# Optimization experiments

Measured on AMD Instinct MI355X. Metric: run time of the kernel, lower is better.

## Reference

```python
import jax, jax.numpy as jnp
import numpy as np

N_NODES = 50000
N_EDGES = 800000
IN_C = 128
OUT_C = 128


def setup_inputs() -> dict:
    key = jax.random.key(0)
    k1, k2, k3 = jax.random.split(key, 3)
    x = jax.random.normal(k1, (N_NODES, IN_C), dtype=jnp.float32)
    edge_index = jax.random.randint(k2, (2, N_EDGES), 0, N_NODES, dtype=jnp.int64)
    weight = jax.random.normal(k3, (IN_C, OUT_C), dtype=jnp.float32) * 0.01
    bias = jnp.zeros((OUT_C,), dtype=jnp.float32)
    return {"x": x, "edge_index": edge_index, "weight": weight, "bias": bias}


def reference(x, edge_index, weight, bias):
    num_nodes = x.shape[0]
    # add self-loops
    loop = jnp.arange(num_nodes, dtype=edge_index.dtype)
    src = jnp.concatenate([edge_index[0], loop])  # [E + N]
    dst = jnp.concatenate([edge_index[1], loop])  # [E + N]
    # in-degree (incl. self-loops) via scatter-add
    deg = jax.ops.segment_sum(jnp.ones_like(dst, dtype=x.dtype), dst,
                              num_segments=num_nodes)
    # deg >= 1 due to self-loops, but guard inf like the original
    deg_inv_sqrt = jnp.where(deg > 0, jax.lax.rsqrt(deg), 0.0)
    norm = deg_inv_sqrt[src] * deg_inv_sqrt[dst]  # [E + N]
    x_transformed = x @ weight  # [N, out_c]
    messages = x_transformed[src] * norm[:, None]  # [E + N, out_c]
    out = jax.ops.segment_sum(messages, dst, num_segments=num_nodes)
    return out + bias
```

## Files before the change

kernel.cpp:

```cpp
#include <hip/hip_runtime.h>

#define C 128
#define CHUNK 3200
#define K4CAP 5120

typedef short bf16x8 __attribute__((ext_vector_type(8)));
typedef float f32x4 __attribute__((ext_vector_type(4)));

__device__ inline unsigned short f2bf(float f) {
    unsigned u = __float_as_uint(f);
    u += 0x7fffu + ((u >> 16) & 1u);
    return (unsigned short)(u >> 16);
}

__device__ inline unsigned pk2bf(float lo, float hi) {
    return (unsigned)f2bf(lo) | ((unsigned)f2bf(hi) << 16);
}

__global__ __launch_bounds__(256) void kfused(
        const int* __restrict__ ei, int e,
        int* __restrict__ cur, unsigned* __restrict__ staging,
        int nblocks, int nbuck,
        const float* __restrict__ W, unsigned short* __restrict__ Wt) {
    int b = blockIdx.x;
    int t = threadIdx.x;
    if (b >= nblocks) {
        int i = (b - nblocks) * 256 + t;
        int nn = i >> 7, k = i & 127;
        Wt[nn * 128 + k] = f2bf(W[k * 128 + nn]);
        return;
    }
    __shared__ int sdst[CHUNK];
    __shared__ int ssrc[CHUNK];
    __shared__ int h[256];
    __shared__ int c[256];
    h[t] = 0;
    __syncthreads();
    int base = b * CHUNK;
    int lim = min(CHUNK, e - base);
    for (int i = t; i < lim; i += 256) {
        int s = ei[base + i];
        int d = ei[e + base + i];
        ssrc[i] = s;
        sdst[i] = d;
        atomicAdd(&h[d >> 8], 1);
    }
    __syncthreads();
    if (t < nbuck) {
        int cnt = h[t];
        c[t] = cnt ? atomicAdd(&cur[t], cnt) : 0;
    }
    __syncthreads();
    for (int i = t; i < lim; i += 256) {
        int s = ssrc[i];
        int d = sdst[i];
        int g = d >> 8;
        int pos = atomicAdd(&c[g], 1);
        if (pos < K4CAP)
            staging[(size_t)g * K4CAP + pos] = (unsigned)s | ((unsigned)(d & 255) << 16);
    }
}

__global__ __launch_bounds__(256) void k4_finalize(
        const unsigned* __restrict__ staging, const int* __restrict__ cur,
        int2* __restrict__ row_se, float* __restrict__ dis,
        unsigned short* __restrict__ srcs, int n) {
    __shared__ unsigned rec[K4CAP];
    __shared__ int sc[256];
    __shared__ int cu[256];
    int g = blockIdx.x, t = threadIdx.x;
    int cnt = min(cur[g], K4CAP);
    int s0 = g * K4CAP;
    sc[t] = 0;
    __syncthreads();
    for (int li = t; li < cnt; li += 256) {
        unsigned r = staging[s0 + li];
        rec[li] = r;
        atomicAdd(&sc[r >> 16], 1);
    }
    __syncthreads();
    int v = sc[t];
    __syncthreads();
    for (int off = 1; off < 256; off <<= 1) {
        int u = (t >= off) ? sc[t - off] : 0;
        __syncthreads();
        sc[t] += u;
        __syncthreads();
    }
    int excl = sc[t] - v;
    int idx = g * 256 + t;
    if (idx < n) {
        row_se[idx] = make_int2(s0 + excl, s0 + excl + v);
        dis[idx] = rsqrtf((float)(v + 1));
    }
    cu[t] = s0 + excl;
    __syncthreads();
    for (int li = t; li < cnt; li += 256) {
        unsigned r = rec[li];
        int pos = atomicAdd(&cu[r >> 16], 1);
        srcs[pos] = (unsigned short)(r & 0xffffu);
    }
}

__global__ __launch_bounds__(256) void gemm_mfma(
        const float* __restrict__ x, const unsigned short* __restrict__ Wt,
        const float* __restrict__ dis, unsigned short* __restrict__ xts, int n) {
    const int lane = threadIdx.x & 63;
    const int wave = threadIdx.x >> 6;
    const int m = lane & 15;
    const int q = lane >> 4;
    const int r0 = blockIdx.x * 64 + wave * 16;
    const int row = r0 + m;
    const int rowc = (row < n) ? row : (n - 1);

    f32x4 acc[8];
#pragma unroll
    for (int nt = 0; nt < 8; ++nt) acc[nt] = (f32x4){0.f, 0.f, 0.f, 0.f};

#pragma unroll
    for (int kb = 0; kb < 4; ++kb) {
        const int k0 = kb * 32 + q * 8;
        const float4* xp = (const float4*)(x + (size_t)rowc * 128 + k0);
        float4 xa = xp[0];
        float4 xb = xp[1];
        union { unsigned u[4]; bf16x8 v; } af;
        af.u[0] = pk2bf(xa.x, xa.y);
        af.u[1] = pk2bf(xa.z, xa.w);
        af.u[2] = pk2bf(xb.x, xb.y);
        af.u[3] = pk2bf(xb.z, xb.w);
#pragma unroll
        for (int nt = 0; nt < 8; ++nt) {
            bf16x8 bf = *(const bf16x8*)(Wt + (size_t)(nt * 16 + m) * 128 + k0);
            acc[nt] = __builtin_amdgcn_mfma_f32_16x16x32_bf16(af.v, bf, acc[nt], 0, 0, 0);
        }
    }

    float dv[4];
    int gr[4];
#pragma unroll
    for (int r = 0; r < 4; ++r) {
        gr[r] = r0 + q * 4 + r;
        dv[r] = dis[(gr[r] < n) ? gr[r] : (n - 1)];
    }
#pragma unroll
    for (int nt = 0; nt < 8; ++nt) {
        int col = nt * 16 + m;
#pragma unroll
        for (int r = 0; r < 4; ++r) {
            if (gr[r] < n)
                xts[(size_t)gr[r] * 128 + col] = f2bf(acc[nt][r] * dv[r]);
        }
    }
}

__device__ inline void acc8(float* a, uint4 w) {
    a[0] += __uint_as_float(w.x << 16);
    a[1] += __uint_as_float(w.x & 0xffff0000u);
    a[2] += __uint_as_float(w.y << 16);
    a[3] += __uint_as_float(w.y & 0xffff0000u);
    a[4] += __uint_as_float(w.z << 16);
    a[5] += __uint_as_float(w.z & 0xffff0000u);
    a[6] += __uint_as_float(w.w << 16);
    a[7] += __uint_as_float(w.w & 0xffff0000u);
}

__global__ void gather4(const int2* __restrict__ row_se,
                        const unsigned short* __restrict__ srcs,
                        const unsigned short* __restrict__ xts,
                        const float* __restrict__ dis,
                        const float* __restrict__ bias, float* __restrict__ out, int n) {
    int node = blockIdx.x * 4 + (threadIdx.x >> 6);
    if (node >= n) return;
    int lane = threadIdx.x & 63;
    int e = lane >> 4, q = lane & 15;
    const uint4* x4 = (const uint4*)xts;
    int2 se = row_se[node];
    int end = se.y;
    float a0[8] = {0, 0, 0, 0, 0, 0, 0, 0};
    float a1[8] = {0, 0, 0, 0, 0, 0, 0, 0};
    if (e == 0) acc8(a0, x4[node * 16 + q]);
    int j = se.x + e;
    for (; j + 4 < end; j += 8) {
        int s0 = srcs[j], s1 = srcs[j + 4];
        uint4 m0 = x4[s0 * 16 + q];
        uint4 m1 = x4[s1 * 16 + q];
        acc8(a0, m0);
        acc8(a1, m1);
    }
    if (j < end) acc8(a0, x4[(int)srcs[j] * 16 + q]);
#pragma unroll
    for (int i = 0; i < 8; ++i) a0[i] += a1[i];
#pragma unroll
    for (int i = 0; i < 8; ++i) {
        a0[i] += __shfl_xor(a0[i], 16, 64);
        a0[i] += __shfl_xor(a0[i], 32, 64);
    }
    float d = dis[node];
    if (e == 0) {
        const float4 b = ((const float4*)bias)[q * 2];
        float4 o;
        o.x = a0[0] * d + b.x;
        o.y = a0[1] * d + b.y;
        o.z = a0[2] * d + b.z;
        o.w = a0[3] * d + b.w;
        ((float4*)(out + (size_t)node * 128))[q * 2] = o;
    } else if (e == 1) {
        const float4 b = ((const float4*)bias)[q * 2 + 1];
        float4 o;
        o.x = a0[4] * d + b.x;
        o.y = a0[5] * d + b.y;
        o.z = a0[6] * d + b.z;
        o.w = a0[7] * d + b.w;
        ((float4*)(out + (size_t)node * 128))[q * 2 + 1] = o;
    }
}

extern "C" void kernel_launch(void* const* d_in, const int* in_sizes, int n_in,
                              void* d_out, int out_size, void* d_ws, size_t ws_size,
                              hipStream_t stream) {
    const float* x    = (const float*)d_in[0];
    const int*   ei   = (const int*)d_in[1];
    const float* W    = (const float*)d_in[2];
    const float* bias = (const float*)d_in[3];
    float* out = (float*)d_out;

    const int n = in_sizes[0] / C;
    const int e = in_sizes[1] / 2;
    const int nblocks = (e + CHUNK - 1) / CHUNK;
    const int nbuck = (n + 255) >> 8;
    const int G = (n + 63) / 64;

    char* p = (char*)d_ws;
    auto alloc = [&](size_t bytes) {
        char* r = p;
        p += (bytes + 15) & ~(size_t)15;
        return (void*)r;
    };
    int*      cur     = (int*)alloc(nbuck * 4);
    unsigned* staging = (unsigned*)alloc((size_t)nbuck * K4CAP * 4);
    int2*     row_se  = (int2*)alloc((size_t)n * 8);
    float*    dis     = (float*)alloc(n * 4);
    unsigned short* srcs = (unsigned short*)alloc((size_t)nbuck * K4CAP * 2);
    unsigned short* xts  = (unsigned short*)alloc((size_t)n * C * 2);
    unsigned short* Wt   = (unsigned short*)alloc(128 * 128 * 2);

    hipMemsetAsync(cur, 0, nbuck * 4, stream);
    kfused<<<nblocks + 64, 256, 0, stream>>>(ei, e, cur, staging, nblocks,
                                             nbuck, W, Wt);
    k4_finalize<<<nbuck, 256, 0, stream>>>(staging, cur, row_se, dis, srcs, n);
    gemm_mfma<<<G, 256, 0, stream>>>(x, Wt, dis, xts, n);
    gather4<<<(n + 3) / 4, 256, 0, stream>>>(row_se, srcs, xts, dis, bias, out, n);
}
```

Measured before the change: 161.8 us.

## Fuse CSR finalize with GEMM and drop global atomics via per-block slots

The bucketing kernel now writes each block's per-bucket counts into fixed-size slots instead of reserving space through global atomics, which removes the memset launch. The finalize and GEMM kernels are merged into one launch with disjoint block ranges, so the GEMM no longer waits on degree computation. Because of that, the source-side normalization moves out of the GEMM epilogue and into the gather loop, which adds one dis load per edge. Risks: slots hold at most 64 edges per bucket per block, edges past that are silently dropped, and finalize threads copy their slots serially.

```diff
diff --git a/kernel.cpp b/kernel.cpp
--- a/kernel.cpp
+++ b/kernel.cpp
@@ -2,6 +2,7 @@
 
 #define C 128
 #define CHUNK 3200
+#define SLOT 64
 #define K4CAP 5120
 
 typedef short bf16x8 __attribute__((ext_vector_type(8)));
@@ -17,9 +18,9 @@
     return (unsigned)f2bf(lo) | ((unsigned)f2bf(hi) << 16);
 }
 
-__global__ __launch_bounds__(256) void kfused(
+__global__ __launch_bounds__(256) void kA(
         const int* __restrict__ ei, int e,
-        int* __restrict__ cur, unsigned* __restrict__ staging,
+        int* __restrict__ cnt, unsigned* __restrict__ staging,
         int nblocks, int nbuck,
         const float* __restrict__ W, unsigned short* __restrict__ Wt) {
     int b = blockIdx.x;
@@ -47,8 +48,8 @@
     }
     __syncthreads();
     if (t < nbuck) {
-        int cnt = h[t];
-        c[t] = cnt ? atomicAdd(&cur[t], cnt) : 0;
+        cnt[t * nblocks + b] = h[t];
+        c[t] = (t * nblocks + b) * SLOT;
     }
     __syncthreads();
     for (int i = t; i < lim; i += 256) {
@@ -56,112 +57,120 @@
         int d = sdst[i];
         int g = d >> 8;
         int pos = atomicAdd(&c[g], 1);
-        if (pos < K4CAP)
-            staging[(size_t)g * K4CAP + pos] = (unsigned)s | ((unsigned)(d & 255) << 16);
-    }
-}
-
-__global__ __launch_bounds__(256) void k4_finalize(
-        const unsigned* __restrict__ staging, const int* __restrict__ cur,
+        if (pos < (g * nblocks + b + 1) * SLOT)
+            staging[pos] = (unsigned)s | ((unsigned)(d & 255) << 16);
+    }
+}
+
+__global__ __launch_bounds__(256) void kB(
+        const unsigned* __restrict__ staging, const int* __restrict__ cnt,
+        int nblocks, int nbuck,
         int2* __restrict__ row_se, float* __restrict__ dis,
-        unsigned short* __restrict__ srcs, int n) {
+        unsigned short* __restrict__ srcs,
+        const float* __restrict__ x, const unsigned short* __restrict__ Wt,
+        unsigned short* __restrict__ xts, int n) {
     __shared__ unsigned rec[K4CAP];
     __shared__ int sc[256];
     __shared__ int cu[256];
-    int g = blockIdx.x, t = threadIdx.x;
-    int cnt = min(cur[g], K4CAP);
-    int s0 = g * K4CAP;
-    sc[t] = 0;
-    __syncthreads();
-    for (int li = t; li < cnt; li += 256) {
-        unsigned r = staging[s0 + li];
-        rec[li] = r;
-        atomicAdd(&sc[r >> 16], 1);
-    }
-    __syncthreads();
-    int v = sc[t];
-    __syncthreads();
-    for (int off = 1; off < 256; off <<= 1) {
-        int u = (t >= off) ? sc[t - off] : 0;
-        __syncthreads();
-        sc[t] += u;
-        __syncthreads();
-    }
-    int excl = sc[t] - v;
-    int idx = g * 256 + t;
-    if (idx < n) {
-        row_se[idx] = make_int2(s0 + excl, s0 + excl + v);
-        dis[idx] = rsqrtf((float)(v + 1));
-    }
-    cu[t] = s0 + excl;
-    __syncthreads();
-    for (int li = t; li < cnt; li += 256) {
-        unsigned r = rec[li];
-        int pos = atomicAdd(&cu[r >> 16], 1);
-        srcs[pos] = (unsigned short)(r & 0xffffu);
-    }
-}
-
-__global__ __launch_bounds__(256) void gemm_mfma(
-        const float* __restrict__ x, const unsigned short* __restrict__ Wt,
-        const float* __restrict__ dis, unsigned short* __restrict__ xts, int n) {
-    const int lane = threadIdx.x & 63;
-    const int wave = threadIdx.x >> 6;
-    const int m = lane & 15;
-    const int q = lane >> 4;
-    const int r0 = blockIdx.x * 64 + wave * 16;
-    const int row = r0 + m;
-    const int rowc = (row < n) ? row : (n - 1);
-
-    f32x4 acc[8];
-#pragma unroll
-    for (int nt = 0; nt < 8; ++nt) acc[nt] = (f32x4){0.f, 0.f, 0.f, 0.f};
-
-#pragma unroll
-    for (int kb = 0; kb < 4; ++kb) {
-        const int k0 = kb * 32 + q * 8;
-        const float4* xp = (const float4*)(x + (size_t)rowc * 128 + k0);
-        float4 xa = xp[0];
-        float4 xb = xp[1];
-        union { unsigned u[4]; bf16x8 v; } af;
-        af.u[0] = pk2bf(xa.x, xa.y);
-        af.u[1] = pk2bf(xa.z, xa.w);
-        af.u[2] = pk2bf(xb.x, xb.y);
-        af.u[3] = pk2bf(xb.z, xb.w);
+    int b = blockIdx.x, t = threadIdx.x;
+    if (b < nbuck) {
+        int g = b;
+        int segc = (t < nblocks) ? cnt[g * nblocks + t] : 0;
+        sc[t] = segc;
+        __syncthreads();
+        for (int off = 1; off < 256; off <<= 1) {
+            int u = (t >= off) ? sc[t - off] : 0;
+            __syncthreads();
+            sc[t] += u;
+            __syncthreads();
+        }
+        int segbase = sc[t] - segc;
+        int total = min(sc[255], K4CAP);
+        const unsigned* segp = staging + ((size_t)g * nblocks + t) * SLOT;
+        for (int k = 0; k < segc; ++k)
+            if (segbase + k < K4CAP) rec[segbase + k] = segp[k];
+        __syncthreads();
+        sc[t] = 0;
+        __syncthreads();
+        for (int li = t; li < total; li += 256)
+            atomicAdd(&sc[rec[li] >> 16], 1);
+        __syncthreads();
+        int v = sc[t];
+        __syncthreads();
+        for (int off = 1; off < 256; off <<= 1) {
+            int u = (t >= off) ? sc[t - off] : 0;
+            __syncthreads();
+            sc[t] += u;
+            __syncthreads();
+        }
+        int excl = sc[t] - v;
+        int idx = g * 256 + t;
+        int s0 = g * K4CAP;
+        if (idx < n) {
+            row_se[idx] = make_int2(s0 + excl, s0 + excl + v);
+            dis[idx] = rsqrtf((float)(v + 1));
+        }
+        cu[t] = s0 + excl;
+        __syncthreads();
+        for (int li = t; li < total; li += 256) {
+            unsigned r = rec[li];
+            int pos = atomicAdd(&cu[r >> 16], 1);
+            srcs[pos] = (unsigned short)(r & 0xffffu);
+        }
+    } else {
+        const int gb = b - nbuck;
+        const int lane = t & 63;
+        const int wave = t >> 6;
+        const int m = lane & 15;
+        const int q = lane >> 4;
+        const int r0 = gb * 64 + wave * 16;
+        const int row = r0 + m;
+        const int rowc = (row < n) ? row : (n - 1);
+
+        f32x4 acc[8];
+#pragma unroll
+        for (int nt = 0; nt < 8; ++nt) acc[nt] = (f32x4){0.f, 0.f, 0.f, 0.f};
+
+#pragma unroll
+        for (int kb = 0; kb < 4; ++kb) {
+            const int k0 = kb * 32 + q * 8;
+            const float4* xp = (const float4*)(x + (size_t)rowc * 128 + k0);
+            float4 xa = xp[0];
+            float4 xb = xp[1];
+            union { unsigned u[4]; bf16x8 v; } af;
+            af.u[0] = pk2bf(xa.x, xa.y);
+            af.u[1] = pk2bf(xa.z, xa.w);
+            af.u[2] = pk2bf(xb.x, xb.y);
+            af.u[3] = pk2bf(xb.z, xb.w);
+#pragma unroll
+            for (int nt = 0; nt < 8; ++nt) {
+                bf16x8 bf = *(const bf16x8*)(Wt + (size_t)(nt * 16 + m) * 128 + k0);
+                acc[nt] = __builtin_amdgcn_mfma_f32_16x16x32_bf16(af.v, bf, acc[nt], 0, 0, 0);
+            }
+        }
+
 #pragma unroll
         for (int nt = 0; nt < 8; ++nt) {
-            bf16x8 bf = *(const bf16x8*)(Wt + (size_t)(nt * 16 + m) * 128 + k0);
-            acc[nt] = __builtin_amdgcn_mfma_f32_16x16x32_bf16(af.v, bf, acc[nt], 0, 0, 0);
-        }
-    }
-
-    float dv[4];
-    int gr[4];
-#pragma unroll
-    for (int r = 0; r < 4; ++r) {
-        gr[r] = r0 + q * 4 + r;
-        dv[r] = dis[(gr[r] < n) ? gr[r] : (n - 1)];
-    }
-#pragma unroll
-    for (int nt = 0; nt < 8; ++nt) {
-        int col = nt * 16 + m;
-#pragma unroll
-        for (int r = 0; r < 4; ++r) {
-            if (gr[r] < n)
-                xts[(size_t)gr[r] * 128 + col] = f2bf(acc[nt][r] * dv[r]);
-        }
-    }
-}
-
-__device__ inline void acc8(float* a, uint4 w) {
-    a[0] += __uint_as_float(w.x << 16);
-    a[1] += __uint_as_float(w.x & 0xffff0000u);
-    a[2] += __uint_as_float(w.y << 16);
-    a[3] += __uint_as_float(w.y & 0xffff0000u);
-    a[4] += __uint_as_float(w.z << 16);
-    a[5] += __uint_as_float(w.z & 0xffff0000u);
-    a[6] += __uint_as_float(w.w << 16);
-    a[7] += __uint_as_float(w.w & 0xffff0000u);
+            int col = nt * 16 + m;
+#pragma unroll
+            for (int r = 0; r < 4; ++r) {
+                int gr = r0 + q * 4 + r;
+                if (gr < n)
+                    xts[(size_t)gr * 128 + col] = f2bf(acc[nt][r]);
+            }
+        }
+    }
+}
+
+__device__ inline void fma8(float* a, uint4 w, float d) {
+    a[0] += __uint_as_float(w.x << 16) * d;
+    a[1] += __uint_as_float(w.x & 0xffff0000u) * d;
+    a[2] += __uint_as_float(w.y << 16) * d;
+    a[3] += __uint_as_float(w.y & 0xffff0000u) * d;
+    a[4] += __uint_as_float(w.z << 16) * d;
+    a[5] += __uint_as_float(w.z & 0xffff0000u) * d;
+    a[6] += __uint_as_float(w.w << 16) * d;
+    a[7] += __uint_as_float(w.w & 0xffff0000u) * d;
 }
 
 __global__ void gather4(const int2* __restrict__ row_se,
@@ -176,18 +185,23 @@
     const uint4* x4 = (const uint4*)xts;
     int2 se = row_se[node];
     int end = se.y;
+    float dself = dis[node];
     float a0[8] = {0, 0, 0, 0, 0, 0, 0, 0};
     float a1[8] = {0, 0, 0, 0, 0, 0, 0, 0};
-    if (e == 0) acc8(a0, x4[node * 16 + q]);
+    if (e == 0) fma8(a0, x4[node * 16 + q], dself);
     int j = se.x + e;
     for (; j + 4 < end; j += 8) {
         int s0 = srcs[j], s1 = srcs[j + 4];
+        float d0 = dis[s0], d1 = dis[s1];
         uint4 m0 = x4[s0 * 16 + q];
         uint4 m1 = x4[s1 * 16 + q];
-        acc8(a0, m0);
-        acc8(a1, m1);
-    }
-    if (j < end) acc8(a0, x4[(int)srcs[j] * 16 + q]);
+        fma8(a0, m0, d0);
+        fma8(a1, m1, d1);
+    }
+    if (j < end) {
+        int s = srcs[j];
+        fma8(a0, x4[s * 16 + q], dis[s]);
+    }
 #pragma unroll
     for (int i = 0; i < 8; ++i) a0[i] += a1[i];
 #pragma unroll
@@ -195,22 +209,21 @@
         a0[i] += __shfl_xor(a0[i], 16, 64);
         a0[i] += __shfl_xor(a0[i], 32, 64);
     }
-    float d = dis[node];
     if (e == 0) {
         const float4 b = ((const float4*)bias)[q * 2];
         float4 o;
-        o.x = a0[0] * d + b.x;
-        o.y = a0[1] * d + b.y;
-        o.z = a0[2] * d + b.z;
-        o.w = a0[3] * d + b.w;
+        o.x = a0[0] * dself + b.x;
+        o.y = a0[1] * dself + b.y;
+        o.z = a0[2] * dself + b.z;
+        o.w = a0[3] * dself + b.w;
         ((float4*)(out + (size_t)node * 128))[q * 2] = o;
     } else if (e == 1) {
         const float4 b = ((const float4*)bias)[q * 2 + 1];
         float4 o;
-        o.x = a0[4] * d + b.x;
-        o.y = a0[5] * d + b.y;
-        o.z = a0[6] * d + b.z;
-        o.w = a0[7] * d + b.w;
+        o.x = a0[4] * dself + b.x;
+        o.y = a0[5] * dself + b.y;
+        o.z = a0[6] * dself + b.z;
+        o.w = a0[7] * dself + b.w;
         ((float4*)(out + (size_t)node * 128))[q * 2 + 1] = o;
     }
 }
@@ -236,18 +249,17 @@
         p += (bytes + 15) & ~(size_t)15;
         return (void*)r;
     };
-    int*      cur     = (int*)alloc(nbuck * 4);
-    unsigned* staging = (unsigned*)alloc((size_t)nbuck * K4CAP * 4);
+    int*      cnt     = (int*)alloc((size_t)nbuck * nblocks * 4);
+    unsigned* staging = (unsigned*)alloc((size_t)nbuck * nblocks * SLOT * 4);
     int2*     row_se  = (int2*)alloc((size_t)n * 8);
     float*    dis     = (float*)alloc(n * 4);
     unsigned short* srcs = (unsigned short*)alloc((size_t)nbuck * K4CAP * 2);
     unsigned short* xts  = (unsigned short*)alloc((size_t)n * C * 2);
     unsigned short* Wt   = (unsigned short*)alloc(128 * 128 * 2);
 
-    hipMemsetAsync(cur, 0, nbuck * 4, stream);
-    kfused<<<nblocks + 64, 256, 0, stream>>>(ei, e, cur, staging, nblocks,
-                                             nbuck, W, Wt);
-    k4_finalize<<<nbuck, 256, 0, stream>>>(staging, cur, row_se, dis, srcs, n);
-    gemm_mfma<<<G, 256, 0, stream>>>(x, Wt, dis, xts, n);
+    kA<<<nblocks + 64, 256, 0, stream>>>(ei, e, cnt, staging, nblocks, nbuck,
+                                         W, Wt);
+    kB<<<nbuck + G, 256, 0, stream>>>(staging, cnt, nblocks, nbuck, row_se,
+                                      dis, srcs, x, Wt, xts, n);
     gather4<<<(n + 3) / 4, 256, 0, stream>>>(row_se, srcs, xts, dis, bias, out, n);
 }
```

Result: faster. 150.3 us (-7.1%).
